# Performance work log

Hardware: AMD Instinct MI355X
Metric: run time of the kernel (lower is better)

The kernel has to match this reference:

```python
import jax, jax.numpy as jnp
import numpy as np

KS = 7
HEADS = 8


def _conv1x1(a, w, b):
    # a: (B,Cin,H,W), w: (Cout,Cin), b: (Cout,)
    return jnp.einsum('bchw,oc->bohw', a, w) + b[None, :, None, None]


def _unfold2d(a, ks):
    # a: (B,C,Hp,Wp) -> (B,C,H,W,ks,ks) sliding windows, stride 1
    H = a.shape[2] - ks + 1
    W = a.shape[3] - ks + 1
    ii = jnp.arange(H)[:, None] + jnp.arange(ks)[None, :]  # (H,ks)
    jj = jnp.arange(W)[:, None] + jnp.arange(ks)[None, :]  # (W,ks)
    return a[:, :, ii[:, None, :, None], jj[None, :, None, :]]


def setup_inputs() -> dict:
    key = jax.random.key(0)
    ks = jax.random.split(key, 10)
    B, C, H, W = 4, 128, 56, 56
    x = jax.random.normal(ks[0], (B, C, H, W), dtype=jnp.float32)
    sc = 1.0 / np.sqrt(C)
    q_w = jax.random.normal(ks[1], (C, C), dtype=jnp.float32) * sc
    q_b = jax.random.normal(ks[2], (C,), dtype=jnp.float32) * 0.01
    k_w = jax.random.normal(ks[3], (C, C), dtype=jnp.float32) * sc
    k_b = jax.random.normal(ks[4], (C,), dtype=jnp.float32) * 0.01
    v_w = jax.random.normal(ks[5], (C, C), dtype=jnp.float32) * sc
    v_b = jax.random.normal(ks[6], (C,), dtype=jnp.float32) * 0.01
    rel_h = jax.random.normal(ks[7], (C // 2, KS, 1), dtype=jnp.float32)
    rel_w = jax.random.normal(ks[8], (C // 2, 1, KS), dtype=jnp.float32)
    return {'x': x, 'q_w': q_w, 'q_b': q_b, 'k_w': k_w, 'k_b': k_b,
            'v_w': v_w, 'v_b': v_b, 'rel_h': rel_h, 'rel_w': rel_w}


def reference(x, q_w, q_b, k_w, k_b, v_w, v_b, rel_h, rel_w):
    B, C, H, W = x.shape
    dkh = C // HEADS
    K2 = KS * KS
    pl = (KS - 1) // 2
    pr = KS - 1 - pl
    xp = jnp.pad(x, ((0, 0), (0, 0), (pl, pr), (pl, pr)))

    k = _conv1x1(xp, k_w, k_b)
    v = _conv1x1(xp, v_w, v_b)
    q = _conv1x1(x, q_w, q_b)

    # unfold K/V into (B,C,H,W,KS,KS) then reshape exactly as torch does
    # (this reshape intermixes channel/window axes; replicated faithfully)
    k6 = _unfold2d(k, KS).reshape(B, HEADS, H, W, dkh, K2)
    v6 = _unfold2d(v, KS).reshape(B, HEADS, H, W, dkh, K2)
    q6 = q.reshape(B, HEADS, H, W, dkh, 1)

    # q^T k over the dkh axis -> (B,heads,H,W,KS,KS)
    qk = jnp.einsum('bhxyd,bhxydk->bhxyk', q6[..., 0], k6)
    qk = qk.reshape(B, HEADS, H, W, KS, KS)

    # einsum 'bhxydz,cij->bhxyij' has no shared index: factorizes as
    # (sum over d,z of q) * (sum over c of rel)
    qsum = q6.sum(axis=(4, 5))  # (B,heads,H,W)
    qk = qk + qsum[..., None, None] * rel_h.sum(axis=0)  # (KS,1) broadcast
    qk = qk + qsum[..., None, None] * rel_w.sum(axis=0)  # (1,KS) broadcast

    w = jax.nn.softmax(qk.reshape(B, HEADS, H, W, K2), axis=-1)
    out = jnp.einsum('bhxyk,bhxydk->bhxyd', w, v6)  # (B,heads,H,W,dvh)
    return out.reshape(B, C, H, W)
```

## Files before the change

### kernel.cpp

```cpp
#include <hip/hip_runtime.h>
#include <hip/hip_bf16.h>
#include <math.h>

#define NB    4
#define NC    128
#define NPIX  3136
#define CHW   401408
#define SKS   68
#define STS   19

template <int CTRL, int RM>
__device__ __forceinline__ float dpp_mov(float x, float old) {
    return __int_as_float(__builtin_amdgcn_update_dpp(
        __float_as_int(old), __float_as_int(x), CTRL, RM, 0xf, false));
}
__device__ __forceinline__ float wave_max(float x) {
    x = fmaxf(x, dpp_mov<0x111, 0xf>(x, x));
    x = fmaxf(x, dpp_mov<0x112, 0xf>(x, x));
    x = fmaxf(x, dpp_mov<0x114, 0xf>(x, x));
    x = fmaxf(x, dpp_mov<0x118, 0xf>(x, x));
    x = fmaxf(x, dpp_mov<0x142, 0xa>(x, x));
    x = fmaxf(x, dpp_mov<0x143, 0xc>(x, x));
    return __int_as_float(__builtin_amdgcn_readlane(__float_as_int(x), 63));
}
__device__ __forceinline__ float wave_sum(float x) {
    x = x + dpp_mov<0x111, 0xf>(x, 0.f);
    x = x + dpp_mov<0x112, 0xf>(x, 0.f);
    x = x + dpp_mov<0x114, 0xf>(x, 0.f);
    x = x + dpp_mov<0x118, 0xf>(x, 0.f);
    x = x + dpp_mov<0x142, 0xa>(x, 0.f);
    x = x + dpp_mov<0x143, 0xc>(x, 0.f);
    return __int_as_float(__builtin_amdgcn_readlane(__float_as_int(x), 63));
}

__global__ __launch_bounds__(256) void prep_kernel(
    const float* __restrict__ qw, const float* __restrict__ kw,
    const float* __restrict__ vw,
    const float* __restrict__ rel_h, const float* __restrict__ rel_w,
    float* __restrict__ w4q, float* __restrict__ w4k, float* __restrict__ w4v,
    float* __restrict__ rb)
{
    int idx = blockIdx.x * 256 + threadIdx.x;
    if (idx < 3 * 16384) {
        int m = idx >> 14;
        int r = idx & 16383;
        int cc = r & 3;
        int t = r >> 2;
        int o = t & 127;
        int c4 = t >> 7;
        const float* src = (m == 0) ? qw : (m == 1) ? kw : vw;
        float* dst = (m == 0) ? w4q : (m == 1) ? w4k : w4v;
        dst[r] = src[o * 128 + c4 * 4 + cc];
    }
    if (idx < 14) {
        const float* src = (idx < 7) ? rel_h : rel_w;
        int off = (idx < 7) ? idx : idx - 7;
        float s = 0.f;
        for (int c = 0; c < 64; ++c) s += src[c * 7 + off];
        rb[idx] = s;
    }
}

__global__ __launch_bounds__(256) void conv_kernel(
    const float* __restrict__ x,
    const float* __restrict__ w4q, const float* __restrict__ w4k,
    const float* __restrict__ w4v,
    const float* __restrict__ qb, const float* __restrict__ kb,
    const float* __restrict__ vb,
    float* __restrict__ q, float* __restrict__ kbuf, float* __restrict__ vbuf)
{
    __shared__ float sx[128 * 16];
    __shared__ float st[3 * 128 * STS];
    int bid = blockIdx.x;
    int tile = bid % 196;
    int b = bid / 196;
    int pix0 = tile * 16;
    const float* xb = x + b * CHW + pix0;

    for (int i = threadIdx.x; i < 512; i += 256) {
        int c = i >> 2, p4 = (i & 3) * 4;
        *(float4*)(sx + c * 16 + p4) = *(const float4*)(xb + c * NPIX + p4);
    }
    __syncthreads();

    int lane = threadIdx.x & 63;
    int wave = threadIdx.x >> 6;
    int o = wave * 32 + (lane & 31);
    int ph = (lane >> 5) * 8;
    const float4* Wq = (const float4*)w4q + o;
    const float4* Wk = (const float4*)w4k + o;
    const float4* Wv = (const float4*)w4v + o;

    float4 wqc = Wq[0], wkc = Wk[0], wvc = Wv[0];
    float aq[8] = {}, ak[8] = {}, av[8] = {};
    #pragma unroll 1
    for (int c4 = 0; c4 < 32; ++c4) {
        float4 xs[8];
        #pragma unroll
        for (int cc = 0; cc < 4; ++cc) {
            xs[2 * cc]     = *(const float4*)(sx + (c4 * 4 + cc) * 16 + ph);
            xs[2 * cc + 1] = *(const float4*)(sx + (c4 * 4 + cc) * 16 + ph + 4);
        }
        float4 wq4 = wqc, wk4 = wkc, wv4 = wvc;
        if (c4 < 31) {
            wqc = Wq[(c4 + 1) * 128];
            wkc = Wk[(c4 + 1) * 128];
            wvc = Wv[(c4 + 1) * 128];
        }
        float wqr[4] = {wq4.x, wq4.y, wq4.z, wq4.w};
        float wkr[4] = {wk4.x, wk4.y, wk4.z, wk4.w};
        float wvr[4] = {wv4.x, wv4.y, wv4.z, wv4.w};
        #pragma unroll
        for (int cc = 0; cc < 4; ++cc) {
            float4 xa = xs[2 * cc], xc = xs[2 * cc + 1];
            float xv[8] = {xa.x, xa.y, xa.z, xa.w, xc.x, xc.y, xc.z, xc.w};
            #pragma unroll
            for (int p = 0; p < 8; ++p) {
                aq[p] += wqr[cc] * xv[p];
                ak[p] += wkr[cc] * xv[p];
                av[p] += wvr[cc] * xv[p];
            }
        }
    }
    float bq = qb[o], bk = kb[o], bv = vb[o];
    float* wrq = st + o * STS + ph;
    float* wrk = st + 128 * STS + o * STS + ph;
    float* wrv = st + 2 * 128 * STS + o * STS + ph;
    #pragma unroll
    for (int p = 0; p < 8; ++p) {
        wrq[p] = aq[p] + bq;
        wrk[p] = ak[p] + bk;
        wrv[p] = av[p] + bv;
    }
    __syncthreads();

    int pix = threadIdx.x & 15;
    int o8 = (threadIdx.x >> 4) * 8;
    float* qd = q + b * CHW + pix0 + pix;
    float* kd = kbuf + b * CHW + pix0 + pix;
    float* vd = vbuf + b * CHW + pix0 + pix;
    #pragma unroll
    for (int i = 0; i < 8; ++i) {
        int r = o8 + i;
        qd[r * NPIX] = st[r * STS + pix];
        kd[r * NPIX] = st[128 * STS + r * STS + pix];
        vd[r * NPIX] = st[2 * 128 * STS + r * STS + pix];
    }
}

__global__ __launch_bounds__(256) void attn_kernel(
    const float* __restrict__ q, const float* __restrict__ kbuf,
    const float* __restrict__ vbuf,
    const float* __restrict__ kb, const float* __restrict__ vb,
    const float* __restrict__ rb, float* __restrict__ out)
{
    __shared__ float sK[20 * SKS];
    __shared__ float sV[21 * SKS];
    __shared__ float sW[4 * 64];
    int bid = blockIdx.x;
    int qpart = bid & 3;
    int bc = bid >> 2;
    int ch = bc & 127;
    const float* qc = q + bc * NPIX + 784 * qpart;
    const float* kc = kbuf + bc * NPIX;
    const float* vc = vbuf + bc * NPIX;
    float* oc = out + bc * NPIX + 784 * qpart;
    float kbias = kb[ch], vbias = vb[ch];
    int qr0 = 14 * qpart;

    for (int i = threadIdx.x; i < 20 * 62; i += 256) {
        int yy = i / 62, xx = i - yy * 62;
        int gy = qr0 + yy - 3;
        int gx = xx - 3;
        bool in = (gy >= 0) && (gy < 56) && (gx >= 0) && (gx < 56);
        int off = in ? gy * 56 + gx : 0;
        float kv = in ? kc[off] : kbias;
        float vv = in ? vc[off] : vbias;
        sK[yy * SKS + xx] = kv;
        sV[yy * SKS + xx] = vv;
    }
    for (int i = threadIdx.x; i < SKS; i += 256) sV[20 * SKS + i] = 0.f;
    __syncthreads();

    int lane = threadIdx.x & 63;
    int wave = threadIdx.x >> 6;
    int k2 = min(lane, 48);
    int di = k2 / 7, dj = k2 - di * 7;
    float rbias = rb[di] + rb[7 + dj];
    int koff = di * SKS + dj;
    int t16 = lane & 15, p = lane >> 4;
    float* sWw = sW + wave * 64;

    int ulu = __builtin_amdgcn_readfirstlane(wave * 16);
    float4 p0 = *(const float4*)(qc + ulu);
    float4 p1 = *(const float4*)(qc + ulu + 4);
    float4 p2 = *(const float4*)(qc + ulu + 8);
    float4 p3 = *(const float4*)(qc + ulu + 12);

    for (int gl = wave; gl < 49; gl += 4) {
        int ul0 = gl * 16;
        int y0 = ul0 / 56;
        int x0 = ul0 - y0 * 56;

        float4 q0 = p0, q1 = p1, q2 = p2, q3 = p3;
        if (gl + 4 < 49) {
            int un = __builtin_amdgcn_readfirstlane((gl + 4) * 16);
            p0 = *(const float4*)(qc + un);
            p1 = *(const float4*)(qc + un + 4);
            p2 = *(const float4*)(qc + un + 8);
            p3 = *(const float4*)(qc + un + 12);
        }
        float qa[16] = {q0.x, q0.y, q0.z, q0.w, q1.x, q1.y, q1.z, q1.w,
                        q2.x, q2.y, q2.z, q2.w, q3.x, q3.y, q3.z, q3.w};
        float qs = 0.f;
        #pragma unroll
        for (int t = 0; t < 16; ++t) qs += qa[t];

        float acc = 0.f;
        const float* kb_ = sK + y0 * SKS + x0 + koff;
        if (x0 != 48) {
            #pragma unroll
            for (int t = 0; t < 16; ++t) acc += qa[t] * kb_[t];
        } else {
            const float* kb2 = sK + (y0 + 1) * SKS + koff;
            #pragma unroll
            for (int t = 0; t < 8; ++t) acc += qa[t] * kb_[t];
            #pragma unroll
            for (int t = 0; t < 8; ++t) acc += qa[8 + t] * kb2[t];
        }
        float val = (lane < 49) ? (acc + qs * rbias) : -1e30f;

        float mS = wave_max(val);
        float e = __expf(val - mS);
        float sS = wave_sum(e);
        float wgt = e * __builtin_amdgcn_rcpf(sS);
        sWw[lane] = wgt;

        int u = ul0 + t16;
        int yt = u / 56;
        int xt = u - yt * 56;
        const float* vbase = sV + yt * SKS + xt + p * (2 * SKS);
        const float* wbase = sWw + p * 14;
        float oacc = 0.f;
        #pragma unroll
        for (int j = 0; j < 7; ++j) oacc += wbase[j] * vbase[j];
        #pragma unroll
        for (int j = 0; j < 7; ++j) oacc += wbase[7 + j] * vbase[SKS + j];
        oacc += __shfl_xor(oacc, 16);
        oacc += __shfl_xor(oacc, 32);
        if (lane < 16) oc[ul0 + lane] = oacc;
    }
}

extern "C" void kernel_launch(void* const* d_in, const int* in_sizes, int n_in,
                              void* d_out, int out_size, void* d_ws, size_t ws_size,
                              hipStream_t stream) {
    const float* x     = (const float*)d_in[0];
    const float* qw    = (const float*)d_in[1];
    const float* qb    = (const float*)d_in[2];
    const float* kw    = (const float*)d_in[3];
    const float* kb    = (const float*)d_in[4];
    const float* vw    = (const float*)d_in[5];
    const float* vb    = (const float*)d_in[6];
    const float* rel_h = (const float*)d_in[7];
    const float* rel_w = (const float*)d_in[8];
    float* out = (float*)d_out;

    float* ws   = (float*)d_ws;
    float* kbuf = ws;
    float* vbuf = kbuf + 1605632;
    float* qbuf = vbuf + 1605632;
    float* w4q  = qbuf + 1605632;
    float* w4k  = w4q + 16384;
    float* w4v  = w4k + 16384;
    float* rb   = w4v + 16384;

    prep_kernel<<<192, 256, 0, stream>>>(qw, kw, vw, rel_h, rel_w,
                                         w4q, w4k, w4v, rb);
    conv_kernel<<<784, 256, 0, stream>>>(x, w4q, w4k, w4v, qb, kb, vb,
                                         qbuf, kbuf, vbuf);
    attn_kernel<<<2048, 256, 0, stream>>>(qbuf, kbuf, vbuf, kb, vb, rb, out);
}
```

Before: 72.24 us.

## Precompute per-group query sums in conv kernel and streamline attention loop

The conv kernel now reduces each 16-pixel group's query values into a sum and writes it to a new workspace buffer. The attention kernel reads that sum instead of recomputing it. The attention loop also replaces per-iteration divisions with incremental coordinate updates, splits accumulators into two chains for ILP, and moves the first q prefetch before the barrier to overlap with the shared-memory fill. The conv inner loop is restructured to double-buffer the weight loads across two channel groups. The cost is an extra global write and read per group, plus a larger workspace.

```diff
diff --git a/kernel.cpp b/kernel.cpp
--- a/kernel.cpp
+++ b/kernel.cpp
@@ -61,13 +61,26 @@
     }
 }
 
+#define CBLK(WQ, WK, WV, ROW) do {                                       \
+    const float* xr = sx + (ROW) * 16 + ph;                              \
+    float4 xa = *(const float4*)xr;                                      \
+    float4 xc = *(const float4*)(xr + 4);                                \
+    float xv[8] = {xa.x, xa.y, xa.z, xa.w, xc.x, xc.y, xc.z, xc.w};      \
+    _Pragma("unroll")                                                    \
+    for (int pp = 0; pp < 8; ++pp) {                                     \
+        aq[pp] += (WQ) * xv[pp];                                         \
+        ak[pp] += (WK) * xv[pp];                                         \
+        av[pp] += (WV) * xv[pp];                                         \
+    } } while (0)
+
 __global__ __launch_bounds__(256) void conv_kernel(
     const float* __restrict__ x,
     const float* __restrict__ w4q, const float* __restrict__ w4k,
     const float* __restrict__ w4v,
     const float* __restrict__ qb, const float* __restrict__ kb,
     const float* __restrict__ vb,
-    float* __restrict__ q, float* __restrict__ kbuf, float* __restrict__ vbuf)
+    float* __restrict__ q, float* __restrict__ kbuf, float* __restrict__ vbuf,
+    float* __restrict__ qsum)
 {
     __shared__ float sx[128 * 16];
     __shared__ float st[3 * 128 * STS];
@@ -91,38 +104,31 @@
     const float4* Wk = (const float4*)w4k + o;
     const float4* Wv = (const float4*)w4v + o;
 
-    float4 wqc = Wq[0], wkc = Wk[0], wvc = Wv[0];
+    float4 wqA = Wq[0],   wkA = Wk[0],   wvA = Wv[0];
+    float4 wqB = Wq[128], wkB = Wk[128], wvB = Wv[128];
     float aq[8] = {}, ak[8] = {}, av[8] = {};
     #pragma unroll 1
-    for (int c4 = 0; c4 < 32; ++c4) {
-        float4 xs[8];
-        #pragma unroll
-        for (int cc = 0; cc < 4; ++cc) {
-            xs[2 * cc]     = *(const float4*)(sx + (c4 * 4 + cc) * 16 + ph);
-            xs[2 * cc + 1] = *(const float4*)(sx + (c4 * 4 + cc) * 16 + ph + 4);
-        }
-        float4 wq4 = wqc, wk4 = wkc, wv4 = wvc;
-        if (c4 < 31) {
-            wqc = Wq[(c4 + 1) * 128];
-            wkc = Wk[(c4 + 1) * 128];
-            wvc = Wv[(c4 + 1) * 128];
-        }
-        float wqr[4] = {wq4.x, wq4.y, wq4.z, wq4.w};
-        float wkr[4] = {wk4.x, wk4.y, wk4.z, wk4.w};
-        float wvr[4] = {wv4.x, wv4.y, wv4.z, wv4.w};
-        #pragma unroll
-        for (int cc = 0; cc < 4; ++cc) {
-            float4 xa = xs[2 * cc], xc = xs[2 * cc + 1];
-            float xv[8] = {xa.x, xa.y, xa.z, xa.w, xc.x, xc.y, xc.z, xc.w};
-            #pragma unroll
-            for (int p = 0; p < 8; ++p) {
-                aq[p] += wqr[cc] * xv[p];
-                ak[p] += wkr[cc] * xv[p];
-                av[p] += wvr[cc] * xv[p];
-            }
-        }
+    for (int c4 = 0; c4 < 32; c4 += 2) {
+        int ia = ((c4 + 2) & 31) * 128;
+        int ib = ((c4 + 3) & 31) * 128;
+        CBLK(wqA.x, wkA.x, wvA.x, c4 * 4 + 0);
+        CBLK(wqA.y, wkA.y, wvA.y, c4 * 4 + 1);
+        CBLK(wqA.z, wkA.z, wvA.z, c4 * 4 + 2);
+        CBLK(wqA.w, wkA.w, wvA.w, c4 * 4 + 3);
+        wqA = Wq[ia]; wkA = Wk[ia]; wvA = Wv[ia];
+        CBLK(wqB.x, wkB.x, wvB.x, c4 * 4 + 4);
+        CBLK(wqB.y, wkB.y, wvB.y, c4 * 4 + 5);
+        CBLK(wqB.z, wkB.z, wvB.z, c4 * 4 + 6);
+        CBLK(wqB.w, wkB.w, wvB.w, c4 * 4 + 7);
+        wqB = Wq[ib]; wkB = Wk[ib]; wvB = Wv[ib];
     }
     float bq = qb[o], bk = kb[o], bv = vb[o];
+
+    float qp = ((aq[0] + aq[1]) + (aq[2] + aq[3]))
+             + ((aq[4] + aq[5]) + (aq[6] + aq[7])) + 8.f * bq;
+    qp += __shfl_xor(qp, 32);
+    if (lane < 32) qsum[(b * 196 + tile) * 128 + wave * 32 + lane] = qp;
+
     float* wrq = st + o * STS + ph;
     float* wrk = st + 128 * STS + o * STS + ph;
     float* wrv = st + 2 * 128 * STS + o * STS + ph;
@@ -150,7 +156,7 @@
 
 __global__ __launch_bounds__(256) void attn_kernel(
     const float* __restrict__ q, const float* __restrict__ kbuf,
-    const float* __restrict__ vbuf,
+    const float* __restrict__ vbuf, const float* __restrict__ qsum,
     const float* __restrict__ kb, const float* __restrict__ vb,
     const float* __restrict__ rb, float* __restrict__ out)
 {
@@ -161,9 +167,11 @@
     int qpart = bid & 3;
     int bc = bid >> 2;
     int ch = bc & 127;
+    int b = bc >> 7;
     const float* qc = q + bc * NPIX + 784 * qpart;
     const float* kc = kbuf + bc * NPIX;
     const float* vc = vbuf + bc * NPIX;
+    const float* qsp = qsum + (b * 196 + qpart * 49) * 128 + ch;
     float* oc = out + bc * NPIX + 784 * qpart;
     float kbias = kb[ch], vbias = vb[ch];
     int qr0 = 14 * qpart;
@@ -180,7 +188,6 @@
         sV[yy * SKS + xx] = vv;
     }
     for (int i = threadIdx.x; i < SKS; i += 256) sV[20 * SKS + i] = 0.f;
-    __syncthreads();
 
     int lane = threadIdx.x & 63;
     int wave = threadIdx.x >> 6;
@@ -191,44 +198,48 @@
     int t16 = lane & 15, p = lane >> 4;
     float* sWw = sW + wave * 64;
 
-    int ulu = __builtin_amdgcn_readfirstlane(wave * 16);
-    float4 p0 = *(const float4*)(qc + ulu);
-    float4 p1 = *(const float4*)(qc + ulu + 4);
-    float4 p2 = *(const float4*)(qc + ulu + 8);
-    float4 p3 = *(const float4*)(qc + ulu + 12);
+    int ul0 = wave * 16;
+    int y0 = 0, x0 = ul0;
+    float4 p0 = *(const float4*)(qc + ul0);
+    float4 p1 = *(const float4*)(qc + ul0 + 4);
+    float4 p2 = *(const float4*)(qc + ul0 + 8);
+    float4 p3 = *(const float4*)(qc + ul0 + 12);
+    float qsP = qsp[wave * 128];
+    __syncthreads();
 
     for (int gl = wave; gl < 49; gl += 4) {
-        int ul0 = gl * 16;
-        int y0 = ul0 / 56;
-        int x0 = ul0 - y0 * 56;
-
-        float4 q0 = p0, q1 = p1, q2 = p2, q3 = p3;
+        float acc0, acc1;
+        const float* kp = sK + y0 * SKS + x0 + koff;
+        if (x0 != 48) {
+            acc0  = p0.x * kp[0];   acc1  = p0.y * kp[1];
+            acc0 += p0.z * kp[2];   acc1 += p0.w * kp[3];
+            acc0 += p1.x * kp[4];   acc1 += p1.y * kp[5];
+            acc0 += p1.z * kp[6];   acc1 += p1.w * kp[7];
+            acc0 += p2.x * kp[8];   acc1 += p2.y * kp[9];
+            acc0 += p2.z * kp[10];  acc1 += p2.w * kp[11];
+            acc0 += p3.x * kp[12];  acc1 += p3.y * kp[13];
+            acc0 += p3.z * kp[14];  acc1 += p3.w * kp[15];
+        } else {
+            const float* kp2 = sK + (y0 + 1) * SKS + koff;
+            acc0  = p0.x * kp[0];   acc1  = p0.y * kp[1];
+            acc0 += p0.z * kp[2];   acc1 += p0.w * kp[3];
+            acc0 += p1.x * kp[4];   acc1 += p1.y * kp[5];
+            acc0 += p1.z * kp[6];   acc1 += p1.w * kp[7];
+            acc0 += p2.x * kp2[0];  acc1 += p2.y * kp2[1];
+            acc0 += p2.z * kp2[2];  acc1 += p2.w * kp2[3];
+            acc0 += p3.x * kp2[4];  acc1 += p3.y * kp2[5];
+            acc0 += p3.z * kp2[6];  acc1 += p3.w * kp2[7];
+        }
+        float val = (lane < 49) ? (acc0 + acc1 + qsP * rbias) : -1e30f;
+
         if (gl + 4 < 49) {
-            int un = __builtin_amdgcn_readfirstlane((gl + 4) * 16);
+            int un = ul0 + 64;
             p0 = *(const float4*)(qc + un);
             p1 = *(const float4*)(qc + un + 4);
             p2 = *(const float4*)(qc + un + 8);
             p3 = *(const float4*)(qc + un + 12);
+            qsP = qsp[(gl + 4) * 128];
         }
-        float qa[16] = {q0.x, q0.y, q0.z, q0.w, q1.x, q1.y, q1.z, q1.w,
-                        q2.x, q2.y, q2.z, q2.w, q3.x, q3.y, q3.z, q3.w};
-        float qs = 0.f;
-        #pragma unroll
-        for (int t = 0; t < 16; ++t) qs += qa[t];
-
-        float acc = 0.f;
-        const float* kb_ = sK + y0 * SKS + x0 + koff;
-        if (x0 != 48) {
-            #pragma unroll
-            for (int t = 0; t < 16; ++t) acc += qa[t] * kb_[t];
-        } else {
-            const float* kb2 = sK + (y0 + 1) * SKS + koff;
-            #pragma unroll
-            for (int t = 0; t < 8; ++t) acc += qa[t] * kb_[t];
-            #pragma unroll
-            for (int t = 0; t < 8; ++t) acc += qa[8 + t] * kb2[t];
-        }
-        float val = (lane < 49) ? (acc + qs * rbias) : -1e30f;
 
         float mS = wave_max(val);
         float e = __expf(val - mS);
@@ -236,19 +247,24 @@
         float wgt = e * __builtin_amdgcn_rcpf(sS);
         sWw[lane] = wgt;
 
-        int u = ul0 + t16;
-        int yt = u / 56;
-        int xt = u - yt * 56;
+        int xt = x0 + t16;
+        int yt = y0;
+        if (xt >= 56) { xt -= 56; ++yt; }
         const float* vbase = sV + yt * SKS + xt + p * (2 * SKS);
         const float* wbase = sWw + p * 14;
-        float oacc = 0.f;
+        float o0 = 0.f, o1 = 0.f;
         #pragma unroll
-        for (int j = 0; j < 7; ++j) oacc += wbase[j] * vbase[j];
+        for (int j = 0; j < 7; ++j) o0 += wbase[j] * vbase[j];
         #pragma unroll
-        for (int j = 0; j < 7; ++j) oacc += wbase[7 + j] * vbase[SKS + j];
+        for (int j = 0; j < 7; ++j) o1 += wbase[7 + j] * vbase[SKS + j];
+        float oacc = o0 + o1;
         oacc += __shfl_xor(oacc, 16);
         oacc += __shfl_xor(oacc, 32);
         if (lane < 16) oc[ul0 + lane] = oacc;
+
+        ul0 += 64;
+        x0 += 8; y0 += 1;
+        if (x0 >= 56) { x0 -= 56; ++y0; }
     }
 }
 
@@ -273,11 +289,12 @@
     float* w4q  = qbuf + 1605632;
     float* w4k  = w4q + 16384;
     float* w4v  = w4k + 16384;
-    float* rb   = w4v + 16384;
+    float* qsm  = w4v + 16384;
+    float* rb   = qsm + 100352;
 
     prep_kernel<<<192, 256, 0, stream>>>(qw, kw, vw, rel_h, rel_w,
                                          w4q, w4k, w4v, rb);
     conv_kernel<<<784, 256, 0, stream>>>(x, w4q, w4k, w4v, qb, kb, vb,
-                                         qbuf, kbuf, vbuf);
-    attn_kernel<<<2048, 256, 0, stream>>>(qbuf, kbuf, vbuf, kb, vb, rb, out);
-}
+                                         qbuf, kbuf, vbuf, qsm);
+    attn_kernel<<<2048, 256, 0, stream>>>(qbuf, kbuf, vbuf, qsm, kb, vb, rb, out);
+}
```

Result: slower. 103.4 us (+43.2%).

## Process two query groups per wave in attention and halve conv pixel tile

Applied to the files above, without the earlier changes.

The attention kernel now has each wave handle two 16-pixel groups per iteration, with fixed-trip loops and a tail group on wave 0. It also splits the dot products into two accumulators and issues the first Q loads before the shared-memory barrier, so reductions overlap and latency is hidden. The conv kernel halves its pixel tile to 8 and doubles its grid, which raises parallelism but reloads the weights twice as often. The changes add register pressure and more hand-written index logic.

```diff
diff --git a/kernel.cpp b/kernel.cpp
--- a/kernel.cpp
+++ b/kernel.cpp
@@ -7,7 +7,8 @@
 #define NPIX  3136
 #define CHW   401408
 #define SKS   68
-#define STS   19
+#define CTS   8
+#define STS   9
 
 template <int CTRL, int RM>
 __device__ __forceinline__ float dpp_mov(float x, float old) {
@@ -31,6 +32,24 @@
     x = x + dpp_mov<0x142, 0xa>(x, 0.f);
     x = x + dpp_mov<0x143, 0xc>(x, 0.f);
     return __int_as_float(__builtin_amdgcn_readlane(__float_as_int(x), 63));
+}
+
+__device__ __forceinline__ float qk16(const float* kp, const float* kp2,
+                                      float4 r0, float4 r1, float4 r2, float4 r3) {
+    float a0, a1;
+    a0  = r0.x * kp[0];   a1  = r0.y * kp[1];
+    a0 += r0.z * kp[2];   a1 += r0.w * kp[3];
+    a0 += r1.x * kp[4];   a1 += r1.y * kp[5];
+    a0 += r1.z * kp[6];   a1 += r1.w * kp[7];
+    a0 += r2.x * kp2[0];  a1 += r2.y * kp2[1];
+    a0 += r2.z * kp2[2];  a1 += r2.w * kp2[3];
+    a0 += r3.x * kp2[4];  a1 += r3.y * kp2[5];
+    a0 += r3.z * kp2[6];  a1 += r3.w * kp2[7];
+    return a0 + a1;
+}
+__device__ __forceinline__ float sum16(float4 r0, float4 r1, float4 r2, float4 r3) {
+    return (((r0.x + r0.y) + (r0.z + r0.w)) + ((r1.x + r1.y) + (r1.z + r1.w)))
+         + (((r2.x + r2.y) + (r2.z + r2.w)) + ((r3.x + r3.y) + (r3.z + r3.w)));
 }
 
 __global__ __launch_bounds__(256) void prep_kernel(
@@ -69,38 +88,36 @@
     const float* __restrict__ vb,
     float* __restrict__ q, float* __restrict__ kbuf, float* __restrict__ vbuf)
 {
-    __shared__ float sx[128 * 16];
+    __shared__ float sx[128 * CTS];
     __shared__ float st[3 * 128 * STS];
     int bid = blockIdx.x;
-    int tile = bid % 196;
-    int b = bid / 196;
-    int pix0 = tile * 16;
+    int tile = bid % 392;
+    int b = bid / 392;
+    int pix0 = tile * CTS;
     const float* xb = x + b * CHW + pix0;
 
-    for (int i = threadIdx.x; i < 512; i += 256) {
-        int c = i >> 2, p4 = (i & 3) * 4;
-        *(float4*)(sx + c * 16 + p4) = *(const float4*)(xb + c * NPIX + p4);
+    {
+        int c = threadIdx.x >> 1, p4 = (threadIdx.x & 1) * 4;
+        *(float4*)(sx + c * CTS + p4) = *(const float4*)(xb + c * NPIX + p4);
     }
     __syncthreads();
 
     int lane = threadIdx.x & 63;
     int wave = threadIdx.x >> 6;
     int o = wave * 32 + (lane & 31);
-    int ph = (lane >> 5) * 8;
+    int ph = (lane >> 5) * 4;
     const float4* Wq = (const float4*)w4q + o;
     const float4* Wk = (const float4*)w4k + o;
     const float4* Wv = (const float4*)w4v + o;
 
     float4 wqc = Wq[0], wkc = Wk[0], wvc = Wv[0];
-    float aq[8] = {}, ak[8] = {}, av[8] = {};
+    float aq[4] = {}, ak[4] = {}, av[4] = {};
     #pragma unroll 1
     for (int c4 = 0; c4 < 32; ++c4) {
-        float4 xs[8];
+        float4 xs[4];
         #pragma unroll
-        for (int cc = 0; cc < 4; ++cc) {
-            xs[2 * cc]     = *(const float4*)(sx + (c4 * 4 + cc) * 16 + ph);
-            xs[2 * cc + 1] = *(const float4*)(sx + (c4 * 4 + cc) * 16 + ph + 4);
-        }
+        for (int cc = 0; cc < 4; ++cc)
+            xs[cc] = *(const float4*)(sx + (c4 * 4 + cc) * CTS + ph);
         float4 wq4 = wqc, wk4 = wkc, wv4 = wvc;
         if (c4 < 31) {
             wqc = Wq[(c4 + 1) * 128];
@@ -112,10 +129,9 @@
         float wvr[4] = {wv4.x, wv4.y, wv4.z, wv4.w};
         #pragma unroll
         for (int cc = 0; cc < 4; ++cc) {
-            float4 xa = xs[2 * cc], xc = xs[2 * cc + 1];
-            float xv[8] = {xa.x, xa.y, xa.z, xa.w, xc.x, xc.y, xc.z, xc.w};
+            float xv[4] = {xs[cc].x, xs[cc].y, xs[cc].z, xs[cc].w};
             #pragma unroll
-            for (int p = 0; p < 8; ++p) {
+            for (int p = 0; p < 4; ++p) {
                 aq[p] += wqr[cc] * xv[p];
                 ak[p] += wkr[cc] * xv[p];
                 av[p] += wvr[cc] * xv[p];
@@ -127,21 +143,21 @@
     float* wrk = st + 128 * STS + o * STS + ph;
     float* wrv = st + 2 * 128 * STS + o * STS + ph;
     #pragma unroll
-    for (int p = 0; p < 8; ++p) {
+    for (int p = 0; p < 4; ++p) {
         wrq[p] = aq[p] + bq;
         wrk[p] = ak[p] + bk;
         wrv[p] = av[p] + bv;
     }
     __syncthreads();
 
-    int pix = threadIdx.x & 15;
-    int o8 = (threadIdx.x >> 4) * 8;
+    int pix = threadIdx.x & 7;
+    int o4 = (threadIdx.x >> 3) * 4;
     float* qd = q + b * CHW + pix0 + pix;
     float* kd = kbuf + b * CHW + pix0 + pix;
     float* vd = vbuf + b * CHW + pix0 + pix;
     #pragma unroll
-    for (int i = 0; i < 8; ++i) {
-        int r = o8 + i;
+    for (int i = 0; i < 4; ++i) {
+        int r = o4 + i;
         qd[r * NPIX] = st[r * STS + pix];
         kd[r * NPIX] = st[128 * STS + r * STS + pix];
         vd[r * NPIX] = st[2 * 128 * STS + r * STS + pix];
@@ -156,7 +172,7 @@
 {
     __shared__ float sK[20 * SKS];
     __shared__ float sV[21 * SKS];
-    __shared__ float sW[4 * 64];
+    __shared__ float sW[4 * 128];
     int bid = blockIdx.x;
     int qpart = bid & 3;
     int bc = bid >> 2;
@@ -180,7 +196,6 @@
         sV[yy * SKS + xx] = vv;
     }
     for (int i = threadIdx.x; i < SKS; i += 256) sV[20 * SKS + i] = 0.f;
-    __syncthreads();
 
     int lane = threadIdx.x & 63;
     int wave = threadIdx.x >> 6;
@@ -189,66 +204,117 @@
     float rbias = rb[di] + rb[7 + dj];
     int koff = di * SKS + dj;
     int t16 = lane & 15, p = lane >> 4;
-    float* sWw = sW + wave * 64;
-
-    int ulu = __builtin_amdgcn_readfirstlane(wave * 16);
-    float4 p0 = *(const float4*)(qc + ulu);
-    float4 p1 = *(const float4*)(qc + ulu + 4);
-    float4 p2 = *(const float4*)(qc + ulu + 8);
-    float4 p3 = *(const float4*)(qc + ulu + 12);
-
-    for (int gl = wave; gl < 49; gl += 4) {
-        int ul0 = gl * 16;
-        int y0 = ul0 / 56;
-        int x0 = ul0 - y0 * 56;
-
-        float4 q0 = p0, q1 = p1, q2 = p2, q3 = p3;
-        if (gl + 4 < 49) {
-            int un = __builtin_amdgcn_readfirstlane((gl + 4) * 16);
-            p0 = *(const float4*)(qc + un);
-            p1 = *(const float4*)(qc + un + 4);
-            p2 = *(const float4*)(qc + un + 8);
-            p3 = *(const float4*)(qc + un + 12);
-        }
-        float qa[16] = {q0.x, q0.y, q0.z, q0.w, q1.x, q1.y, q1.z, q1.w,
-                        q2.x, q2.y, q2.z, q2.w, q3.x, q3.y, q3.z, q3.w};
-        float qs = 0.f;
+    float* sWA = sW + wave * 128;
+    float* sWB = sWA + 64;
+
+    int ulA = wave * 32;
+    int y0 = (ulA >= 56) ? 1 : 0;
+    int x0 = ulA - y0 * 56;
+    float4 a0 = *(const float4*)(qc + ulA);
+    float4 a1 = *(const float4*)(qc + ulA + 4);
+    float4 a2 = *(const float4*)(qc + ulA + 8);
+    float4 a3 = *(const float4*)(qc + ulA + 12);
+    float4 b0 = *(const float4*)(qc + ulA + 16);
+    float4 b1 = *(const float4*)(qc + ulA + 20);
+    float4 b2 = *(const float4*)(qc + ulA + 24);
+    float4 b3 = *(const float4*)(qc + ulA + 28);
+    __syncthreads();
+
+    #pragma unroll 1
+    for (int it = 0; it < 6; ++it) {
+        int xB = x0 + 16, yB = y0;
+        if (xB >= 56) { xB -= 56; ++yB; }
+
+        const float* kpA = sK + y0 * SKS + x0 + koff;
+        const float* kpA2 = (x0 == 48) ? (sK + (y0 + 1) * SKS + koff) : (kpA + 8);
+        const float* kpB = sK + yB * SKS + xB + koff;
+        const float* kpB2 = (xB == 48) ? (sK + (yB + 1) * SKS + koff) : (kpB + 8);
+
+        float qsA = sum16(a0, a1, a2, a3);
+        float qsB = sum16(b0, b1, b2, b3);
+        float accA = qk16(kpA, kpA2, a0, a1, a2, a3);
+        float accB = qk16(kpB, kpB2, b0, b1, b2, b3);
+        float valA = (lane < 49) ? (accA + qsA * rbias) : -1e30f;
+        float valB = (lane < 49) ? (accB + qsB * rbias) : -1e30f;
+
+        int ulCur = ulA;
+        if (it < 5) {
+            int un = ulA + 128;
+            a0 = *(const float4*)(qc + un);
+            a1 = *(const float4*)(qc + un + 4);
+            a2 = *(const float4*)(qc + un + 8);
+            a3 = *(const float4*)(qc + un + 12);
+            b0 = *(const float4*)(qc + un + 16);
+            b1 = *(const float4*)(qc + un + 20);
+            b2 = *(const float4*)(qc + un + 24);
+            b3 = *(const float4*)(qc + un + 28);
+        } else if (wave == 0) {
+            a0 = *(const float4*)(qc + 768);
+            a1 = *(const float4*)(qc + 772);
+            a2 = *(const float4*)(qc + 776);
+            a3 = *(const float4*)(qc + 780);
+        }
+
+        float mA = wave_max(valA);
+        float mB = wave_max(valB);
+        float eA = __expf(valA - mA);
+        float eB = __expf(valB - mB);
+        float sA = wave_sum(eA);
+        float sB = wave_sum(eB);
+        sWA[lane] = eA * __builtin_amdgcn_rcpf(sA);
+        sWB[lane] = eB * __builtin_amdgcn_rcpf(sB);
+
+        int xtA = x0 + t16, ytA = y0;
+        if (xtA >= 56) { xtA -= 56; ++ytA; }
+        int xtB = xB + t16, ytB = yB;
+        if (xtB >= 56) { xtB -= 56; ++ytB; }
+        const float* vbA = sV + ytA * SKS + xtA + p * (2 * SKS);
+        const float* vbB = sV + ytB * SKS + xtB + p * (2 * SKS);
+        const float* wbA = sWA + p * 14;
+        const float* wbB = sWB + p * 14;
+        float oA0 = 0.f, oA1 = 0.f, oB0 = 0.f, oB1 = 0.f;
         #pragma unroll
-        for (int t = 0; t < 16; ++t) qs += qa[t];
-
-        float acc = 0.f;
-        const float* kb_ = sK + y0 * SKS + x0 + koff;
-        if (x0 != 48) {
-            #pragma unroll
-            for (int t = 0; t < 16; ++t) acc += qa[t] * kb_[t];
-        } else {
-            const float* kb2 = sK + (y0 + 1) * SKS + koff;
-            #pragma unroll
-            for (int t = 0; t < 8; ++t) acc += qa[t] * kb_[t];
-            #pragma unroll
-            for (int t = 0; t < 8; ++t) acc += qa[8 + t] * kb2[t];
-        }
+        for (int j = 0; j < 7; ++j) {
+            oA0 += wbA[j] * vbA[j];
+            oB0 += wbB[j] * vbB[j];
+            oA1 += wbA[7 + j] * vbA[SKS + j];
+            oB1 += wbB[7 + j] * vbB[SKS + j];
+        }
+        float oaccA = oA0 + oA1, oaccB = oB0 + oB1;
+        oaccA += __shfl_xor(oaccA, 16);
+        oaccB += __shfl_xor(oaccB, 16);
+        oaccA += __shfl_xor(oaccA, 32);
+        oaccB += __shfl_xor(oaccB, 32);
+        if (lane < 16) {
+            oc[ulCur + lane] = oaccA;
+            oc[ulCur + 16 + lane] = oaccB;
+        }
+
+        ulA += 128; x0 += 16; y0 += 2;
+        if (x0 >= 56) { x0 -= 56; ++y0; }
+    }
+
+    if (wave == 0) {
+        const float* kp = sK + 13 * SKS + 40 + koff;
+        float qs = sum16(a0, a1, a2, a3);
+        float acc = qk16(kp, kp + 8, a0, a1, a2, a3);
         float val = (lane < 49) ? (acc + qs * rbias) : -1e30f;
-
-        float mS = wave_max(val);
-        float e = __expf(val - mS);
-        float sS = wave_sum(e);
-        float wgt = e * __builtin_amdgcn_rcpf(sS);
-        sWw[lane] = wgt;
-
-        int u = ul0 + t16;
-        int yt = u / 56;
-        int xt = u - yt * 56;
-        const float* vbase = sV + yt * SKS + xt + p * (2 * SKS);
-        const float* wbase = sWw + p * 14;
-        float oacc = 0.f;
+        float m = wave_max(val);
+        float e = __expf(val - m);
+        float s = wave_sum(e);
+        sWA[lane] = e * __builtin_amdgcn_rcpf(s);
+        const float* vb_ = sV + 13 * SKS + 40 + t16 + p * (2 * SKS);
+        const float* wb_ = sWA + p * 14;
+        float o0 = 0.f, o1 = 0.f;
         #pragma unroll
-        for (int j = 0; j < 7; ++j) oacc += wbase[j] * vbase[j];
-        #pragma unroll
-        for (int j = 0; j < 7; ++j) oacc += wbase[7 + j] * vbase[SKS + j];
+        for (int j = 0; j < 7; ++j) {
+            o0 += wb_[j] * vb_[j];
+            o1 += wb_[7 + j] * vb_[SKS + j];
+        }
+        float oacc = o0 + o1;
         oacc += __shfl_xor(oacc, 16);
         oacc += __shfl_xor(oacc, 32);
-        if (lane < 16) oc[ul0 + lane] = oacc;
+        if (lane < 16) oc[768 + lane] = oacc;
     }
 }
 
@@ -277,7 +343,7 @@
 
     prep_kernel<<<192, 256, 0, stream>>>(qw, kw, vw, rel_h, rel_w,
                                          w4q, w4k, w4v, rb);
-    conv_kernel<<<784, 256, 0, stream>>>(x, w4q, w4k, w4v, qb, kb, vb,
-                                         qbuf, kbuf, vbuf);
+    conv_kernel<<<1568, 256, 0, stream>>>(x, w4q, w4k, w4v, qb, kb, vb,
+                                          qbuf, kbuf, vbuf);
     attn_kernel<<<2048, 256, 0, stream>>>(qbuf, kbuf, vbuf, kb, vb, rb, out);
 }
```

New measurement: 78.23 us. 1.08x slower.

## Split conv output channels across two blocks and streamline attention loop indexing

Applied to the files above, without the earlier changes.

The 1x1 conv kernel now splits its 128 output channels across two blocks, doubling the grid to 1568 blocks, with 4 pixels per thread instead of 8. This lowers register pressure and shared memory per block in exchange for loading the x tile twice. Weight prefetch is double-buffered two channel-groups ahead. In the attention kernel, the first q loads are issued before the barrier, the per-iteration division is replaced by incremental x/y tracking, and the output dot product is split into two accumulators to shorten the dependency chain.

```diff
diff --git a/kernel.cpp b/kernel.cpp
--- a/kernel.cpp
+++ b/kernel.cpp
@@ -70,10 +70,11 @@
     float* __restrict__ q, float* __restrict__ kbuf, float* __restrict__ vbuf)
 {
     __shared__ float sx[128 * 16];
-    __shared__ float st[3 * 128 * STS];
+    __shared__ float st[3 * 64 * STS];
     int bid = blockIdx.x;
-    int tile = bid % 196;
-    int b = bid / 196;
+    int osplit = bid & 1;
+    int tile = (bid >> 1) % 196;
+    int b = bid / 392;
     int pix0 = tile * 16;
     const float* xb = x + b * CHW + pix0;
 
@@ -85,49 +86,67 @@
 
     int lane = threadIdx.x & 63;
     int wave = threadIdx.x >> 6;
-    int o = wave * 32 + (lane & 31);
-    int ph = (lane >> 5) * 8;
+    int olocal = (wave & 1) * 32 + (lane & 31);
+    int o = osplit * 64 + olocal;
+    int ph = ((wave >> 1) * 2 + (lane >> 5)) * 4;
     const float4* Wq = (const float4*)w4q + o;
     const float4* Wk = (const float4*)w4k + o;
     const float4* Wv = (const float4*)w4v + o;
 
-    float4 wqc = Wq[0], wkc = Wk[0], wvc = Wv[0];
-    float aq[8] = {}, ak[8] = {}, av[8] = {};
+    float4 wqA = Wq[0],   wkA = Wk[0],   wvA = Wv[0];
+    float4 wqB = Wq[128], wkB = Wk[128], wvB = Wv[128];
+    float aq[4] = {}, ak[4] = {}, av[4] = {};
     #pragma unroll 1
-    for (int c4 = 0; c4 < 32; ++c4) {
-        float4 xs[8];
-        #pragma unroll
-        for (int cc = 0; cc < 4; ++cc) {
-            xs[2 * cc]     = *(const float4*)(sx + (c4 * 4 + cc) * 16 + ph);
-            xs[2 * cc + 1] = *(const float4*)(sx + (c4 * 4 + cc) * 16 + ph + 4);
-        }
-        float4 wq4 = wqc, wk4 = wkc, wv4 = wvc;
-        if (c4 < 31) {
-            wqc = Wq[(c4 + 1) * 128];
-            wkc = Wk[(c4 + 1) * 128];
-            wvc = Wv[(c4 + 1) * 128];
-        }
-        float wqr[4] = {wq4.x, wq4.y, wq4.z, wq4.w};
-        float wkr[4] = {wk4.x, wk4.y, wk4.z, wk4.w};
-        float wvr[4] = {wv4.x, wv4.y, wv4.z, wv4.w};
-        #pragma unroll
-        for (int cc = 0; cc < 4; ++cc) {
-            float4 xa = xs[2 * cc], xc = xs[2 * cc + 1];
-            float xv[8] = {xa.x, xa.y, xa.z, xa.w, xc.x, xc.y, xc.z, xc.w};
-            #pragma unroll
-            for (int p = 0; p < 8; ++p) {
-                aq[p] += wqr[cc] * xv[p];
-                ak[p] += wkr[cc] * xv[p];
-                av[p] += wvr[cc] * xv[p];
+    for (int c4 = 0; c4 < 32; c4 += 2) {
+        int ia = ((c4 + 2) & 31) * 128;
+        int ib = ((c4 + 3) & 31) * 128;
+        {
+            float4 xs[4];
+            #pragma unroll
+            for (int r = 0; r < 4; ++r)
+                xs[r] = *(const float4*)(sx + (c4 * 4 + r) * 16 + ph);
+            float wqr[4] = {wqA.x, wqA.y, wqA.z, wqA.w};
+            float wkr[4] = {wkA.x, wkA.y, wkA.z, wkA.w};
+            float wvr[4] = {wvA.x, wvA.y, wvA.z, wvA.w};
+            #pragma unroll
+            for (int cc = 0; cc < 4; ++cc) {
+                float xv[4] = {xs[cc].x, xs[cc].y, xs[cc].z, xs[cc].w};
+                #pragma unroll
+                for (int p = 0; p < 4; ++p) {
+                    aq[p] += wqr[cc] * xv[p];
+                    ak[p] += wkr[cc] * xv[p];
+                    av[p] += wvr[cc] * xv[p];
+                }
             }
         }
+        wqA = Wq[ia]; wkA = Wk[ia]; wvA = Wv[ia];
+        {
+            float4 xs[4];
+            #pragma unroll
+            for (int r = 0; r < 4; ++r)
+                xs[r] = *(const float4*)(sx + (c4 * 4 + 4 + r) * 16 + ph);
+            float wqr[4] = {wqB.x, wqB.y, wqB.z, wqB.w};
+            float wkr[4] = {wkB.x, wkB.y, wkB.z, wkB.w};
+            float wvr[4] = {wvB.x, wvB.y, wvB.z, wvB.w};
+            #pragma unroll
+            for (int cc = 0; cc < 4; ++cc) {
+                float xv[4] = {xs[cc].x, xs[cc].y, xs[cc].z, xs[cc].w};
+                #pragma unroll
+                for (int p = 0; p < 4; ++p) {
+                    aq[p] += wqr[cc] * xv[p];
+                    ak[p] += wkr[cc] * xv[p];
+                    av[p] += wvr[cc] * xv[p];
+                }
+            }
+        }
+        wqB = Wq[ib]; wkB = Wk[ib]; wvB = Wv[ib];
     }
     float bq = qb[o], bk = kb[o], bv = vb[o];
-    float* wrq = st + o * STS + ph;
-    float* wrk = st + 128 * STS + o * STS + ph;
-    float* wrv = st + 2 * 128 * STS + o * STS + ph;
+    float* wrq = st + olocal * STS + ph;
+    float* wrk = st + 64 * STS + olocal * STS + ph;
+    float* wrv = st + 2 * 64 * STS + olocal * STS + ph;
     #pragma unroll
-    for (int p = 0; p < 8; ++p) {
+    for (int p = 0; p < 4; ++p) {
         wrq[p] = aq[p] + bq;
         wrk[p] = ak[p] + bk;
         wrv[p] = av[p] + bv;
@@ -135,16 +154,17 @@
     __syncthreads();
 
     int pix = threadIdx.x & 15;
-    int o8 = (threadIdx.x >> 4) * 8;
-    float* qd = q + b * CHW + pix0 + pix;
-    float* kd = kbuf + b * CHW + pix0 + pix;
-    float* vd = vbuf + b * CHW + pix0 + pix;
+    int r4 = (threadIdx.x >> 4) * 4;
+    int obase = osplit * 64;
+    float* qd = q + b * CHW + obase * NPIX + pix0 + pix;
+    float* kd = kbuf + b * CHW + obase * NPIX + pix0 + pix;
+    float* vd = vbuf + b * CHW + obase * NPIX + pix0 + pix;
     #pragma unroll
-    for (int i = 0; i < 8; ++i) {
-        int r = o8 + i;
+    for (int i = 0; i < 4; ++i) {
+        int r = r4 + i;
         qd[r * NPIX] = st[r * STS + pix];
-        kd[r * NPIX] = st[128 * STS + r * STS + pix];
-        vd[r * NPIX] = st[2 * 128 * STS + r * STS + pix];
+        kd[r * NPIX] = st[64 * STS + r * STS + pix];
+        vd[r * NPIX] = st[2 * 64 * STS + r * STS + pix];
     }
 }
 
@@ -180,7 +200,6 @@
         sV[yy * SKS + xx] = vv;
     }
     for (int i = threadIdx.x; i < SKS; i += 256) sV[20 * SKS + i] = 0.f;
-    __syncthreads();
 
     int lane = threadIdx.x & 63;
     int wave = threadIdx.x >> 6;
@@ -191,20 +210,18 @@
     int t16 = lane & 15, p = lane >> 4;
     float* sWw = sW + wave * 64;
 
-    int ulu = __builtin_amdgcn_readfirstlane(wave * 16);
-    float4 p0 = *(const float4*)(qc + ulu);
-    float4 p1 = *(const float4*)(qc + ulu + 4);
-    float4 p2 = *(const float4*)(qc + ulu + 8);
-    float4 p3 = *(const float4*)(qc + ulu + 12);
+    int ul0 = wave * 16;
+    int y0 = 0, x0 = ul0;
+    float4 p0 = *(const float4*)(qc + ul0);
+    float4 p1 = *(const float4*)(qc + ul0 + 4);
+    float4 p2 = *(const float4*)(qc + ul0 + 8);
+    float4 p3 = *(const float4*)(qc + ul0 + 12);
+    __syncthreads();
 
     for (int gl = wave; gl < 49; gl += 4) {
-        int ul0 = gl * 16;
-        int y0 = ul0 / 56;
-        int x0 = ul0 - y0 * 56;
-
         float4 q0 = p0, q1 = p1, q2 = p2, q3 = p3;
         if (gl + 4 < 49) {
-            int un = __builtin_amdgcn_readfirstlane((gl + 4) * 16);
+            int un = ul0 + 64;
             p0 = *(const float4*)(qc + un);
             p1 = *(const float4*)(qc + un + 4);
             p2 = *(const float4*)(qc + un + 8);
@@ -241,14 +258,19 @@
         int xt = u - yt * 56;
         const float* vbase = sV + yt * SKS + xt + p * (2 * SKS);
         const float* wbase = sWw + p * 14;
-        float oacc = 0.f;
+        float o0 = 0.f, o1 = 0.f;
         #pragma unroll
-        for (int j = 0; j < 7; ++j) oacc += wbase[j] * vbase[j];
+        for (int j = 0; j < 7; ++j) o0 += wbase[j] * vbase[j];
         #pragma unroll
-        for (int j = 0; j < 7; ++j) oacc += wbase[7 + j] * vbase[SKS + j];
+        for (int j = 0; j < 7; ++j) o1 += wbase[7 + j] * vbase[SKS + j];
+        float oacc = o0 + o1;
         oacc += __shfl_xor(oacc, 16);
         oacc += __shfl_xor(oacc, 32);
         if (lane < 16) oc[ul0 + lane] = oacc;
+
+        ul0 += 64;
+        x0 += 8; y0 += 1;
+        if (x0 >= 56) { x0 -= 56; ++y0; }
     }
 }
 
@@ -277,7 +299,7 @@
 
     prep_kernel<<<192, 256, 0, stream>>>(qw, kw, vw, rel_h, rel_w,
                                          w4q, w4k, w4v, rb);
-    conv_kernel<<<784, 256, 0, stream>>>(x, w4q, w4k, w4v, qb, kb, vb,
-                                         qbuf, kbuf, vbuf);
+    conv_kernel<<<1568, 256, 0, stream>>>(x, w4q, w4k, w4v, qb, kb, vb,
+                                          qbuf, kbuf, vbuf);
     attn_kernel<<<2048, 256, 0, stream>>>(qbuf, kbuf, vbuf, kb, vb, rb, out);
 }
```

Result: slower. 138.7 us (+91.9%).
